# Optimization experiments

Measured on AMD Instinct MI355X. Metric: run time of the kernel, lower is better.

Reference implementation:

```python
import jax, jax.numpy as jnp
import numpy as np
from jax import lax

NEG = -1e30  # log-space 'zero' (avoid -inf for mixed-precision safety)
EPS = 1e-7   # keras backend epsilon used in ctc_batch_cost


def setup_inputs() -> dict:
    key = jax.random.key(0)
    k1, k2 = jax.random.split(key)
    B, T, L, V = 64, 1024, 128, 512
    # labels in [0, V-2]; blank index is V-1 (keras ctc_batch_cost convention)
    y_true = jax.random.randint(k1, (B, L), 0, V - 1, dtype=jnp.int64)
    # y_pred are softmax probabilities (ctc_batch_cost logs them internally)
    y_pred = jax.random.uniform(k2, (B, T, V), dtype=jnp.float32)
    y_pred = y_pred / jnp.sum(y_pred, axis=-1, keepdims=True)
    return {"y_true": y_true, "y_pred": y_pred}


def _ctc_loss(y_true, y_pred):
    # y_true: [B, L] int labels; y_pred: [B, T, V] probabilities
    B, T, V = y_pred.shape
    L = y_true.shape[1]
    blank = V - 1
    S = 2 * L + 1  # extended label length: blank,l1,blank,l2,...,blank

    logp = jnp.log(y_pred + EPS)  # [B, T, V]

    # extended label sequence per batch row
    ext = jnp.full((B, S), blank, dtype=y_true.dtype)
    ext = ext.at[:, 1::2].set(y_true)  # [B, S]

    # gather log-probs of extended labels at every time step -> [B, T, S]
    idx = jnp.broadcast_to(ext[:, None, :], (B, T, S))
    lp = jnp.take_along_axis(logp, idx, axis=2)

    # skip transition s-2 -> s allowed iff ext[s] != blank and ext[s] != ext[s-2]
    prev2 = jnp.concatenate([jnp.full((B, 2), -1, dtype=ext.dtype), ext[:, :-2]], axis=1)
    allow_skip = (ext != blank) & (ext != prev2)  # [B, S]

    # init alpha at t=0: only states 0 (blank) and 1 (first label) reachable
    alpha0 = jnp.full((B, S), NEG, dtype=logp.dtype)
    alpha0 = alpha0.at[:, 0].set(lp[:, 0, 0]).at[:, 1].set(lp[:, 0, 1])

    pad1 = jnp.full((B, 1), NEG, dtype=logp.dtype)
    pad2 = jnp.full((B, 2), NEG, dtype=logp.dtype)

    def step(alpha, lp_t):  # alpha, lp_t: [B, S]
        a1 = jnp.concatenate([pad1, alpha[:, :-1]], axis=1)
        a2 = jnp.concatenate([pad2, alpha[:, :-2]], axis=1)
        a2 = jnp.where(allow_skip, a2, NEG)
        new = jnp.logaddexp(jnp.logaddexp(alpha, a1), a2) + lp_t
        return new, None

    lp_rest = jnp.moveaxis(lp[:, 1:], 1, 0)  # [T-1, B, S], time-major for scan
    alpha_T, _ = lax.scan(step, alpha0, lp_rest)

    # total prob ends in last blank or last label
    log_p = jnp.logaddexp(alpha_T[:, -1], alpha_T[:, -2])  # [B]
    return -log_p[:, None]  # [B, 1] like keras ctc_batch_cost


def reference(y_true, y_pred):
    return _ctc_loss(y_true, y_pred)
```

## Files before the change

### kernel.cpp

```cpp
#include <hip/hip_runtime.h>
#include <hip/hip_bf16.h>
#include <cstdint>


#define CTC_B 64
#define CTC_T 1024
#define CTC_L 128
#define CTC_V 512
#define BLANK (CTC_V - 1)
#define EPSF 1e-7f
#define LN2F 0.69314718055994530942f

#define CHUNK 32
#define NCH   (CTC_T / CHUNK)
#define SLOTW 128
#define BIASE 60

__device__ __forceinline__ void gld_lds(const float* g, float* l) {
    __builtin_amdgcn_global_load_lds(
        (const __attribute__((address_space(1))) unsigned int*)g,
        (__attribute__((address_space(3))) unsigned int*)l,
        4, 0, 0);
}

template<int CTRL>
__device__ __forceinline__ float dpp_mov0(float v) {
    int r = __builtin_amdgcn_update_dpp(0, __float_as_int(v), CTRL, 0xf, 0xf, false);
    return __int_as_float(r);
}
template<int CTRL>
__device__ __forceinline__ float dpp_max(float v) {
    int r = __builtin_amdgcn_update_dpp(__float_as_int(v), __float_as_int(v),
                                        CTRL, 0xf, 0xf, false);
    return fmaxf(v, __int_as_float(r));
}

__global__ __launch_bounds__(256, 1)
void ctc_fwd_dpp(const int* __restrict__ y_true,
                 const float* __restrict__ y_pred,
                 float* __restrict__ out) {
    __shared__ __align__(16) float ring[2 * CHUNK * SLOTW];
    __shared__ __align__(16) float blk[CTC_T];

    const int b = blockIdx.x;
    const int tid = threadIdx.x;
    const int wave = tid >> 6;
    const int lane = tid & 63;
    const float* __restrict__ yb = y_pred + (size_t)b * CTC_T * CTC_V;

    if (wave != 0) {
        const int labLo = y_true[b * CTC_L + lane];
        const int labHi = y_true[b * CTC_L + 64 + lane];
        for (int k = wave - 1; k < CTC_T / 64; k += 3)
            gld_lds(yb + (size_t)(64 * k + lane) * CTC_V + BLANK, &blk[64 * k]);
        for (int l = wave - 1; l < CHUNK; l += 3) {
            const float* row = yb + (size_t)l * CTC_V;
            float* slot = &ring[l * SLOTW];
            gld_lds(row + labLo, slot);
            gld_lds(row + labHi, slot + 64);
        }
        __syncthreads();
        for (int c = 0; c < NCH; ++c) {
            if (c + 1 < NCH) {
                const int base = ((c + 1) & 1) * (CHUNK * SLOTW);
                const int t0n = (c + 1) * CHUNK;
                for (int l = wave - 1; l < CHUNK; l += 3) {
                    const float* row = yb + (size_t)(t0n + l) * CTC_V;
                    float* slot = &ring[base + l * SLOTW];
                    gld_lds(row + labLo, slot);
                    gld_lds(row + labHi, slot + 64);
                }
            }
            __syncthreads();
        }
        return;
    }

    const int labA = y_true[b * CTC_L + 2 * lane];
    const int labB = y_true[b * CTC_L + 2 * lane + 1];
    const int labPrev = __shfl_up(labB, 1);
    const float msk1 = (labA != labPrev) ? 1.0f : 0.0f;
    const float msk3 = (labB != labA) ? 1.0f : 0.0f;

    float a0 = 0.0f, a1 = 0.0f, a2 = 0.0f, a3 = 0.0f, a4 = 0.0f;
    float curScale = 1.0f;
    int curE = 0, Eacc = 0;

    float2 qA0, qA1, qA2, qA3, qB0, qB1, qB2, qB3, qC0, qC1, qC2, qC3;
    float  bA0, bA1, bA2, bA3, bB0, bB1, bB2, bB3, bC0, bC1, bC2, bC3;

#define LD2(s_) (*(const float2*)&ring[sb + (s_) * SLOTW + 2 * lane])
#define BL(tt_) (blk[tt_])

#define LOADG(S, l_) do {                                                  \
        q##S##0 = LD2((l_));     q##S##1 = LD2((l_) + 1);                  \
        q##S##2 = LD2((l_) + 2); q##S##3 = LD2((l_) + 3);                  \
        b##S##0 = BL(t0 + (l_));     b##S##1 = BL(t0 + (l_) + 1);          \
        b##S##2 = BL(t0 + (l_) + 2); b##S##3 = BL(t0 + (l_) + 3);          \
    } while (0)

#define DOSTEP(qv, bv) do {                                                \
        const float pb_ = (bv) + EPSF;                                     \
        const float pA_ = (qv).x + EPSF;                                   \
        const float pB_ = (qv).y + EPSF;                                   \
        const float pm1_ = dpp_mov0<0x138>(a3);   \
        const float n0_ = (a0 + pm1_) * pb_;                               \
        const float n1_ = fmaf(msk1, pm1_, a0 + a1) * pA_;                 \
        const float n2_ = (a1 + a2) * pb_;                                 \
        const float n3_ = fmaf(msk3, a1, a2 + a3) * pB_;                   \
        const float n4_ = (a3 + a4) * pb_;                                 \
        a0 = n0_; a1 = n1_; a2 = n2_; a3 = n3_; a4 = n4_;                  \
    } while (0)

#define DORN() do {                                                        \
        a0 *= curScale; a1 *= curScale; a2 *= curScale;                    \
        a3 *= curScale; a4 *= curScale;                                    \
        Eacc += curE;                                                      \
        float m_ = fmaxf(fmaxf(fmaxf(a0, a1), fmaxf(a2, a3)), a4);         \
        m_ = dpp_max<0x111>(m_);                           \
        m_ = dpp_max<0x112>(m_);                           \
        m_ = dpp_max<0x114>(m_);                           \
        m_ = dpp_max<0x118>(m_);                           \
        m_ = dpp_max<0x142>(m_);                         \
        m_ = dpp_max<0x143>(m_);                         \
        const int mb_ = __builtin_amdgcn_readlane(__float_as_int(m_), 63); \
        const int e_ = (mb_ >> 23) & 255;                                  \
        int k_ = 127 + BIASE + 127 - e_;                                   \
        k_ = k_ > 254 ? 254 : (k_ < 1 ? 1 : k_);                           \
        curScale = __int_as_float((unsigned)k_ << 23);                     \
        curE = 127 - k_;                                                   \
    } while (0)

#define PROC4(S) do {                                                      \
        DOSTEP(q##S##0, b##S##0); DOSTEP(q##S##1, b##S##1);                \
        DOSTEP(q##S##2, b##S##2); DOSTEP(q##S##3, b##S##3);                \
    } while (0)
#define PROC4_RN(S) do {                                                   \
        DOSTEP(q##S##0, b##S##0); DORN();                                  \
        DOSTEP(q##S##1, b##S##1);                                          \
        DOSTEP(q##S##2, b##S##2); DOSTEP(q##S##3, b##S##3);                \
    } while (0)

    __syncthreads();

    for (int c = 0; c < NCH; ++c) {
        const int sb = (c & 1) * (CHUNK * SLOTW);
        const int t0 = c * CHUNK;
        if (c == 0) {
            const float pb0 = BL(0) + EPSF;
            const float pl0 = ring[0] + EPSF;
            a0 = (lane == 0) ? pb0 : 0.0f;
            a1 = (lane == 0) ? pl0 : 0.0f;
            LOADG(A, 0); LOADG(B, 4); LOADG(C, 8);
            DOSTEP(qA1, bA1); DOSTEP(qA2, bA2); DOSTEP(qA3, bA3);
            LOADG(A, 12);
            PROC4_RN(B); LOADG(B, 16);
            PROC4_RN(C); LOADG(C, 20);
            PROC4_RN(A); LOADG(A, 24);
            PROC4_RN(B); LOADG(B, 28);
            PROC4_RN(C);
            PROC4_RN(A);
            PROC4_RN(B);
        } else {
            LOADG(A, 0); LOADG(B, 4); LOADG(C, 8);
            PROC4_RN(A); LOADG(A, 12);
            PROC4_RN(B); LOADG(B, 16);
            PROC4_RN(C); LOADG(C, 20);
            PROC4_RN(A); LOADG(A, 24);
            PROC4_RN(B); LOADG(B, 28);
            PROC4_RN(C);
            PROC4_RN(A);
            PROC4_RN(B);
        }
        __syncthreads();
    }

    if (lane == 63) {
        out[b] = -(logf(a3 + a4) + (float)Eacc * LN2F);
    }

#undef PROC4_RN
#undef PROC4
#undef DORN
#undef DOSTEP
#undef LOADG
#undef BL
#undef LD2
}

extern "C" void kernel_launch(void* const* d_in, const int* in_sizes, int n_in,
                              void* d_out, int out_size, void* d_ws, size_t ws_size,
                              hipStream_t stream) {
    (void)in_sizes; (void)n_in; (void)d_ws; (void)ws_size; (void)out_size;
    const int* y_true = (const int*)d_in[0];
    const float* y_pred = (const float*)d_in[1];
    float* out = (float*)d_out;

    ctc_fwd_dpp<<<CTC_B, 256, 0, stream>>>(y_true, y_pred, out);
}
```

Baseline: 63.68 us.

## Stream full y_pred rows into 4-deep LDS ring with 16-byte async loads

Producer waves now copy whole 512-float rows per time step into a 4-buffer LDS ring using 16-byte global_load_lds, replacing the per-label 4-byte gathers and the separate blank preload. The consumer wave gathers labA, labB and blank from LDS. Chunks shrink to 16 steps, prefetch runs three chunks ahead, and explicit vmcnt waits with raw s_barrier replace __syncthreads. This trades coalesced wide loads and deeper prefetch for moving about 4x more bytes from HBM and doing random LDS reads that may bank-conflict.

```diff
diff --git a/kernel.cpp b/kernel.cpp
--- a/kernel.cpp
+++ b/kernel.cpp
@@ -11,16 +11,16 @@
 #define EPSF 1e-7f
 #define LN2F 0.69314718055994530942f
 
-#define CHUNK 32
+#define CHUNK 16
+#define NBUF  4
 #define NCH   (CTC_T / CHUNK)
-#define SLOTW 128
 #define BIASE 60
 
-__device__ __forceinline__ void gld_lds(const float* g, float* l) {
+__device__ __forceinline__ void gld_lds16(const float* g, float* l) {
     __builtin_amdgcn_global_load_lds(
         (const __attribute__((address_space(1))) unsigned int*)g,
         (__attribute__((address_space(3))) unsigned int*)l,
-        4, 0, 0);
+        16, 0, 0);
 }
 
 template<int CTRL>
@@ -36,11 +36,10 @@
 }
 
 __global__ __launch_bounds__(256, 1)
-void ctc_fwd_dpp(const int* __restrict__ y_true,
-                 const float* __restrict__ y_pred,
-                 float* __restrict__ out) {
-    __shared__ __align__(16) float ring[2 * CHUNK * SLOTW];
-    __shared__ __align__(16) float blk[CTC_T];
+void ctc_fwd_stream(const int* __restrict__ y_true,
+                    const float* __restrict__ y_pred,
+                    float* __restrict__ out) {
+    __shared__ __align__(16) float rows[NBUF][CHUNK][CTC_V];
 
     const int b = blockIdx.x;
     const int tid = threadIdx.x;
@@ -49,31 +48,40 @@
     const float* __restrict__ yb = y_pred + (size_t)b * CTC_T * CTC_V;
 
     if (wave != 0) {
-        const int labLo = y_true[b * CTC_L + lane];
-        const int labHi = y_true[b * CTC_L + 64 + lane];
-        for (int k = wave - 1; k < CTC_T / 64; k += 3)
-            gld_lds(yb + (size_t)(64 * k + lane) * CTC_V + BLANK, &blk[64 * k]);
-        for (int l = wave - 1; l < CHUNK; l += 3) {
-            const float* row = yb + (size_t)l * CTC_V;
-            float* slot = &ring[l * SLOTW];
-            gld_lds(row + labLo, slot);
-            gld_lds(row + labHi, slot + 64);
-        }
-        __syncthreads();
+        const int w = wave - 1;
+#define ISSUE(c_) do {                                                     \
+            const int t0_ = (c_) * CHUNK;                                  \
+            float* bufb_ = &rows[(c_) & (NBUF - 1)][0][0];                 \
+            for (int l_ = w; l_ < CHUNK; l_ += 3) {                        \
+                const float* g_ = yb + (size_t)(t0_ + l_) * CTC_V + lane * 4; \
+                float* d_ = bufb_ + l_ * CTC_V;                            \
+                gld_lds16(g_, d_);                                         \
+                gld_lds16(g_ + 256, d_ + 256);                             \
+            }                                                              \
+        } while (0)
+
+        ISSUE(0); ISSUE(1); ISSUE(2);
+        if (w == 0) asm volatile("s_waitcnt vmcnt(24)" ::: "memory");
+        else        asm volatile("s_waitcnt vmcnt(20)" ::: "memory");
+        __builtin_amdgcn_s_barrier();
+        __builtin_amdgcn_sched_barrier(0);
+
         for (int c = 0; c < NCH; ++c) {
-            if (c + 1 < NCH) {
-                const int base = ((c + 1) & 1) * (CHUNK * SLOTW);
-                const int t0n = (c + 1) * CHUNK;
-                for (int l = wave - 1; l < CHUNK; l += 3) {
-                    const float* row = yb + (size_t)(t0n + l) * CTC_V;
-                    float* slot = &ring[base + l * SLOTW];
-                    gld_lds(row + labLo, slot);
-                    gld_lds(row + labHi, slot + 64);
-                }
+            if (c + 3 < NCH) ISSUE(c + 3);
+            if (c <= NCH - 4) {
+                if (w == 0) asm volatile("s_waitcnt vmcnt(24)" ::: "memory");
+                else        asm volatile("s_waitcnt vmcnt(20)" ::: "memory");
+            } else if (c == NCH - 3) {
+                if (w == 0) asm volatile("s_waitcnt vmcnt(12)" ::: "memory");
+                else        asm volatile("s_waitcnt vmcnt(10)" ::: "memory");
+            } else if (c == NCH - 2) {
+                asm volatile("s_waitcnt vmcnt(0)" ::: "memory");
             }
-            __syncthreads();
+            __builtin_amdgcn_s_barrier();
+            __builtin_amdgcn_sched_barrier(0);
         }
         return;
+#undef ISSUE
     }
 
     const int labA = y_true[b * CTC_L + 2 * lane];
@@ -86,24 +94,26 @@
     float curScale = 1.0f;
     int curE = 0, Eacc = 0;
 
-    float2 qA0, qA1, qA2, qA3, qB0, qB1, qB2, qB3, qC0, qC1, qC2, qC3;
-    float  bA0, bA1, bA2, bA3, bB0, bB1, bB2, bB3, bC0, bC1, bC2, bC3;
-
-#define LD2(s_) (*(const float2*)&ring[sb + (s_) * SLOTW + 2 * lane])
-#define BL(tt_) (blk[tt_])
+    float pAA0, pBA0, blA0, pAA1, pBA1, blA1, pAA2, pBA2, blA2, pAA3, pBA3, blA3;
+    float pAB0, pBB0, blB0, pAB1, pBB1, blB1, pAB2, pBB2, blB2, pAB3, pBB3, blB3;
+    float pAC0, pBC0, blC0, pAC1, pBC1, blC1, pAC2, pBC2, blC2, pAC3, pBC3, blC3;
 
 #define LOADG(S, l_) do {                                                  \
-        q##S##0 = LD2((l_));     q##S##1 = LD2((l_) + 1);                  \
-        q##S##2 = LD2((l_) + 2); q##S##3 = LD2((l_) + 3);                  \
-        b##S##0 = BL(t0 + (l_));     b##S##1 = BL(t0 + (l_) + 1);          \
-        b##S##2 = BL(t0 + (l_) + 2); b##S##3 = BL(t0 + (l_) + 3);          \
+        const float* r0_ = bufc + ((l_) + 0) * CTC_V;                      \
+        const float* r1_ = bufc + ((l_) + 1) * CTC_V;                      \
+        const float* r2_ = bufc + ((l_) + 2) * CTC_V;                      \
+        const float* r3_ = bufc + ((l_) + 3) * CTC_V;                      \
+        pA##S##0 = r0_[labA]; pB##S##0 = r0_[labB]; bl##S##0 = r0_[BLANK]; \
+        pA##S##1 = r1_[labA]; pB##S##1 = r1_[labB]; bl##S##1 = r1_[BLANK]; \
+        pA##S##2 = r2_[labA]; pB##S##2 = r2_[labB]; bl##S##2 = r2_[BLANK]; \
+        pA##S##3 = r3_[labA]; pB##S##3 = r3_[labB]; bl##S##3 = r3_[BLANK]; \
     } while (0)
 
-#define DOSTEP(qv, bv) do {                                                \
-        const float pb_ = (bv) + EPSF;                                     \
-        const float pA_ = (qv).x + EPSF;                                   \
-        const float pB_ = (qv).y + EPSF;                                   \
-        const float pm1_ = dpp_mov0<0x138>(a3);   \
+#define DOSTEP(S, k) do {                                                  \
+        const float pb_ = bl##S##k + EPSF;                                 \
+        const float pA_ = pA##S##k + EPSF;                                 \
+        const float pB_ = pB##S##k + EPSF;                                 \
+        const float pm1_ = dpp_mov0<0x138>(a3);  \
         const float n0_ = (a0 + pm1_) * pb_;                               \
         const float n1_ = fmaf(msk1, pm1_, a0 + a1) * pA_;                 \
         const float n2_ = (a1 + a2) * pb_;                                 \
@@ -131,48 +141,34 @@
         curE = 127 - k_;                                                   \
     } while (0)
 
-#define PROC4(S) do {                                                      \
-        DOSTEP(q##S##0, b##S##0); DOSTEP(q##S##1, b##S##1);                \
-        DOSTEP(q##S##2, b##S##2); DOSTEP(q##S##3, b##S##3);                \
-    } while (0)
 #define PROC4_RN(S) do {                                                   \
-        DOSTEP(q##S##0, b##S##0); DORN();                                  \
-        DOSTEP(q##S##1, b##S##1);                                          \
-        DOSTEP(q##S##2, b##S##2); DOSTEP(q##S##3, b##S##3);                \
+        DOSTEP(S, 0); DORN();                                              \
+        DOSTEP(S, 1); DOSTEP(S, 2); DOSTEP(S, 3);                          \
     } while (0)
 
-    __syncthreads();
+    __builtin_amdgcn_s_barrier();
+    __builtin_amdgcn_sched_barrier(0);
 
     for (int c = 0; c < NCH; ++c) {
-        const int sb = (c & 1) * (CHUNK * SLOTW);
-        const int t0 = c * CHUNK;
+        const float* bufc = &rows[c & (NBUF - 1)][0][0];
         if (c == 0) {
-            const float pb0 = BL(0) + EPSF;
-            const float pl0 = ring[0] + EPSF;
+            const float pb0 = bufc[BLANK] + EPSF;
+            const float plA = bufc[labA] + EPSF;
+            LOADG(A, 0); LOADG(B, 4); LOADG(C, 8);
             a0 = (lane == 0) ? pb0 : 0.0f;
-            a1 = (lane == 0) ? pl0 : 0.0f;
-            LOADG(A, 0); LOADG(B, 4); LOADG(C, 8);
-            DOSTEP(qA1, bA1); DOSTEP(qA2, bA2); DOSTEP(qA3, bA3);
+            a1 = (lane == 0) ? plA : 0.0f;
+            DOSTEP(A, 1); DOSTEP(A, 2); DOSTEP(A, 3);
             LOADG(A, 12);
-            PROC4_RN(B); LOADG(B, 16);
-            PROC4_RN(C); LOADG(C, 20);
-            PROC4_RN(A); LOADG(A, 24);
-            PROC4_RN(B); LOADG(B, 28);
+            PROC4_RN(B);
             PROC4_RN(C);
             PROC4_RN(A);
-            PROC4_RN(B);
         } else {
             LOADG(A, 0); LOADG(B, 4); LOADG(C, 8);
             PROC4_RN(A); LOADG(A, 12);
-            PROC4_RN(B); LOADG(B, 16);
-            PROC4_RN(C); LOADG(C, 20);
-            PROC4_RN(A); LOADG(A, 24);
-            PROC4_RN(B); LOADG(B, 28);
-            PROC4_RN(C);
-            PROC4_RN(A);
-            PROC4_RN(B);
+            PROC4_RN(B); PROC4_RN(C); PROC4_RN(A);
         }
-        __syncthreads();
+        __builtin_amdgcn_s_barrier();
+        __builtin_amdgcn_sched_barrier(0);
     }
 
     if (lane == 63) {
@@ -180,12 +176,9 @@
     }
 
 #undef PROC4_RN
-#undef PROC4
 #undef DORN
 #undef DOSTEP
 #undef LOADG
-#undef BL
-#undef LD2
 }
 
 extern "C" void kernel_launch(void* const* d_in, const int* in_sizes, int n_in,
@@ -196,5 +189,5 @@
     const float* y_pred = (const float*)d_in[1];
     float* out = (float*)d_out;
 
-    ctc_fwd_dpp<<<CTC_B, 256, 0, stream>>>(y_true, y_pred, out);
+    ctc_fwd_stream<<<CTC_B, 256, 0, stream>>>(y_true, y_pred, out);
 }
```

Result: slower. 71.42 us (+12.2%).
